# Performance work log

Measured on AMD Instinct MI355X. Metric: run time of the kernel, lower is better.

Reference implementation:

```python
import jax, jax.numpy as jnp
import numpy as np
from jax import lax

NMS_THRESH = 0.5
BN_EPS = 1e-5
TO_REMOVE = 1.0  # neural-motifs box convention (+1 in width/height)


def nms_overlaps(boxes):
    # boxes: [N, C, 4] xyxy -> per-class pairwise IoU [N, N, C]
    x1 = jnp.maximum(boxes[:, None, :, 0], boxes[None, :, :, 0])
    y1 = jnp.maximum(boxes[:, None, :, 1], boxes[None, :, :, 1])
    x2 = jnp.minimum(boxes[:, None, :, 2], boxes[None, :, :, 2])
    y2 = jnp.minimum(boxes[:, None, :, 3], boxes[None, :, :, 3])
    inter = jnp.clip(x2 - x1 + TO_REMOVE, 0.0) * jnp.clip(y2 - y1 + TO_REMOVE, 0.0)
    area = (boxes[:, :, 2] - boxes[:, :, 0] + TO_REMOVE) * (boxes[:, :, 3] - boxes[:, :, 1] + TO_REMOVE)  # [N,C]
    union = area[:, None, :] + area[None, :, :] - inter
    return inter / union


def greedy_nms_labels(obj_dists, is_overlap):
    # faithful port of nms_per_cls: iterative argmax + per-class suppression
    N, C = obj_dists.shape
    scores = jax.nn.softmax(obj_dists, axis=-1)
    scores = scores.at[:, 0].set(-1.0)  # kill background column

    def step(carry, _):
        scores, labels = carry
        flat = jnp.argmax(scores)          # row-major, same as np.unravel_index
        box_ind = flat // C
        cls_ind = flat % C
        labels = labels.at[box_ind].set(cls_ind.astype(jnp.int32))
        ov = is_overlap[box_ind, :, cls_ind]  # [N] bool
        col = jnp.where(ov, 0.0, scores[:, cls_ind])
        scores = scores.at[:, cls_ind].set(col)
        scores = scores.at[box_ind, :].set(-1.0)
        return (scores, labels), None

    (_, labels), _ = lax.scan(step, (scores, jnp.zeros(N, jnp.int32)), None, length=N)
    return labels


def setup_inputs() -> dict:
    key = jax.random.key(0)
    ks = jax.random.split(key, 16)
    N, C, D, E, H, P = 400, 151, 4096, 200, 512, 128
    x = jax.random.normal(ks[0], (N, D), jnp.float32)
    predict_logits = jax.random.normal(ks[1], (N, C), jnp.float32) * 2.0
    pos_input = jax.random.uniform(ks[2], (N, 9), jnp.float32)
    xy = jax.random.uniform(ks[3], (N, C, 2), jnp.float32) * 800.0
    wh = jax.random.uniform(ks[4], (N, C, 2), jnp.float32) * 200.0 + 1.0
    boxes_per_cls = jnp.concatenate([xy, xy + wh], axis=-1)
    sc = lambda k, sh: jax.random.normal(k, sh, jnp.float32) * np.float32(1.0 / np.sqrt(sh[0]))
    return {
        'x': x,
        'predict_logits': predict_logits,
        'pos_input': pos_input,
        'boxes_per_cls': boxes_per_cls,
        'obj_embed_w': jax.random.normal(ks[5], (C, E), jnp.float32) * 0.1,
        'obj_embed2_w': jax.random.normal(ks[6], (C, E), jnp.float32) * 0.1,
        'w_pos1': sc(ks[7], (9, 32)), 'b_pos1': jnp.zeros(32, jnp.float32),
        'bn_gamma': jnp.ones(32, jnp.float32), 'bn_beta': jnp.zeros(32, jnp.float32),
        'bn_mean': jnp.zeros(32, jnp.float32), 'bn_var': jnp.ones(32, jnp.float32),
        'w_pos2': sc(ks[8], (32, P)), 'b_pos2': jnp.zeros(P, jnp.float32),
        'w_lin': sc(ks[9], (D + E + P, H)), 'b_lin': jnp.zeros(H, jnp.float32),
        'w_out': sc(ks[10], (H, C)), 'b_out': jnp.zeros(C, jnp.float32),
        'w_fc': sc(ks[11], (D + E + P, H)), 'b_fc': jnp.zeros(H, jnp.float32),
    }


def reference(x, predict_logits, pos_input, boxes_per_cls, obj_embed_w, obj_embed2_w,
              w_pos1, b_pos1, bn_gamma, bn_beta, bn_mean, bn_var, w_pos2, b_pos2,
              w_lin, b_lin, w_out, b_out, w_fc, b_fc):
    # sgdet inference path of VTransEFeaturePE.forward
    obj_embed = jax.nn.softmax(predict_logits, axis=-1) @ obj_embed_w           # [N,E]
    h = pos_input @ w_pos1 + b_pos1                                             # Linear(9,32)
    h = (h - bn_mean) / jnp.sqrt(bn_var + BN_EPS) * bn_gamma + bn_beta          # BN eval
    pos_embed = jax.nn.relu(h @ w_pos2 + b_pos2)                                # [N,128]
    rep = jnp.concatenate([x, obj_embed, pos_embed], axis=-1)                   # [N,4424]
    obj_dists = (rep @ w_lin + b_lin) @ w_out + b_out                           # [N,C]
    is_overlap = nms_overlaps(boxes_per_cls) >= NMS_THRESH                      # [N,N,C]
    obj_preds = greedy_nms_labels(obj_dists, is_overlap)                        # [N] int32
    obj_embed2 = obj_embed2_w[obj_preds]                                        # [N,E]
    obj_rel_rep = jnp.concatenate([x, pos_embed, obj_embed2], axis=-1)
    edge_ctx = jax.nn.relu(obj_rel_rep @ w_fc + b_fc)                           # [N,H]
    return (obj_dists, obj_preds, edge_ctx)
```

## Files before the change

kernel.cpp:

```cpp
#include <hip/hip_runtime.h>
#include <hip/hip_bf16.h>
#include <stdint.h>

#define NB 400
#define NC 151
#define DX 4096
#define DE 200
#define DP 128
#define DH 512
#define KREP 4424
#define TAILW 328
#define MPAD 416
#define SPLITK 8
#define TILES1 139
#define TILES2 132
#define SLOTS 7
#define SKSTRIDE 152

__device__ __forceinline__ uint32_t f2ord(float f) {
  uint32_t u = __float_as_uint(f);
  return (u & 0x80000000u) ? ~u : (u | 0x80000000u);
}

__global__ __launch_bounds__(256) void k_embed(
    const float* __restrict__ logits, const float* __restrict__ obj_embed_w,
    const float* __restrict__ pos_input, const float* __restrict__ w_pos1,
    const float* __restrict__ b_pos1, const float* __restrict__ bn_gamma,
    const float* __restrict__ bn_beta, const float* __restrict__ bn_mean,
    const float* __restrict__ bn_var, const float* __restrict__ w_pos2,
    const float* __restrict__ b_pos2, float* __restrict__ tail1) {
  int r = blockIdx.x, t = threadIdx.x;
  if (r >= NB) {
    if (t < TAILW) tail1[r * TAILW + t] = 0.f;
    return;
  }
  __shared__ float p[NC];
  __shared__ float red[256];
  __shared__ float hb[32];

  float v = (t < NC) ? logits[r * NC + t] : -INFINITY;
  red[t] = v; __syncthreads();
  for (int s = 128; s > 0; s >>= 1) { if (t < s) red[t] = fmaxf(red[t], red[t + s]); __syncthreads(); }
  float m = red[0]; __syncthreads();
  float e = (t < NC) ? expf(v - m) : 0.f;
  red[t] = e; __syncthreads();
  for (int s = 128; s > 0; s >>= 1) { if (t < s) red[t] += red[t + s]; __syncthreads(); }
  float sum = red[0];
  if (t < NC) p[t] = e / sum;

  if (t < 32) {
    float acc = b_pos1[t];
    for (int k = 0; k < 9; k++) acc += pos_input[r * 9 + k] * w_pos1[k * 32 + t];
    acc = (acc - bn_mean[t]) / sqrtf(bn_var[t] + 1e-5f) * bn_gamma[t] + bn_beta[t];
    hb[t] = acc;
  }
  __syncthreads();

  if (t < DE) {
    float acc = 0.f;
    for (int k = 0; k < NC; k++) acc += p[k] * obj_embed_w[k * DE + t];
    tail1[r * TAILW + t] = acc;
  }
  if (t < DP) {
    float acc = b_pos2[t];
    for (int k = 0; k < 32; k++) acc += hb[k] * w_pos2[k * DP + t];
    tail1[r * TAILW + DE + t] = fmaxf(acc, 0.f);
  }
}

__device__ __forceinline__ void gemm_body(
    const float* __restrict__ x, const float* __restrict__ tail,
    const float* __restrict__ w, float* __restrict__ part,
    int bid, int tiles, int toff) {
  __shared__ __align__(16) float As[32][36];
  __shared__ __align__(16) float Bs[32][68];
  int tid = threadIdx.x;
  int n0 = (bid & 7) * 64, m0 = ((bid >> 3) % 13) * 32;
  int z = bid / 104;
  int tbeg = (z * tiles) / SPLITK, tend = ((z + 1) * tiles) / SPLITK;
  int ty = tid >> 4, tx = tid & 15;
  int a_r = tid >> 3, a_c = (tid & 7) << 2;
  int b_r = tid >> 4, b_c = (tid & 15) << 2;
  float4 acc0 = {0, 0, 0, 0}, acc1 = {0, 0, 0, 0};

  auto loadA = [&](int t) -> float4 {
    int k = t * 32 + a_c;
    int row = m0 + a_r;
    float4 v = {0, 0, 0, 0};
    if (k < KREP) {
      if (k < DX) { if (row < NB) v = *(const float4*)&x[(size_t)row * DX + k]; }
      else v = *(const float4*)&tail[row * TAILW + toff + (k - DX)];
    }
    return v;
  };
  auto loadB = [&](int t, int roff) -> float4 {
    int k = t * 32 + b_r + roff;
    float4 v = {0, 0, 0, 0};
    if (k < KREP) v = *(const float4*)&w[(size_t)k * DH + n0 + b_c];
    return v;
  };

  float4 pa = loadA(tbeg), pb0 = loadB(tbeg, 0), pb1 = loadB(tbeg, 16);
  for (int t = tbeg; t < tend; t++) {
    __syncthreads();
    *(float4*)&As[a_r][a_c] = pa;
    *(float4*)&Bs[b_r][b_c] = pb0;
    *(float4*)&Bs[b_r + 16][b_c] = pb1;
    __syncthreads();
    if (t + 1 < tend) { pa = loadA(t + 1); pb0 = loadB(t + 1, 0); pb1 = loadB(t + 1, 16); }
#pragma unroll
    for (int k4 = 0; k4 < 8; k4++) {
      float4 a0 = *(float4*)&As[ty * 2][k4 * 4];
      float4 a1 = *(float4*)&As[ty * 2 + 1][k4 * 4];
#pragma unroll
      for (int j = 0; j < 4; j++) {
        float4 bv = *(float4*)&Bs[k4 * 4 + j][tx * 4];
        float av0 = (&a0.x)[j], av1 = (&a1.x)[j];
        acc0.x += av0 * bv.x; acc0.y += av0 * bv.y; acc0.z += av0 * bv.z; acc0.w += av0 * bv.w;
        acc1.x += av1 * bv.x; acc1.y += av1 * bv.y; acc1.z += av1 * bv.z; acc1.w += av1 * bv.w;
      }
    }
  }
  int row0 = m0 + ty * 2, col = n0 + tx * 4;
  float* base = part + (size_t)z * NB * DH;
  if (row0 < NB)     *(float4*)&base[row0 * DH + col] = acc0;
  if (row0 + 1 < NB) *(float4*)&base[(row0 + 1) * DH + col] = acc1;
}

__global__ __launch_bounds__(256) void k_g1ov(
    const float* __restrict__ x, const float* __restrict__ tail1,
    const float* __restrict__ w_lin, float* __restrict__ part,
    const float* __restrict__ boxes, uint64_t* __restrict__ ov_bits) {
  int bid = blockIdx.x;
  if (bid >= 832) {
    int c = bid - 832;
    int t = threadIdx.x;
    __shared__ float4 bx[NB];
    const float4* bp4 = (const float4*)boxes;
    for (int j = t; j < NB; j += 256) bx[j] = bp4[j * NC + c];
    __syncthreads();
    int wave = t >> 6, lane = t & 63;
    for (int b = wave; b < NB; b += 4) {
      float4 A = bx[b];
      float areaA = (A.z - A.x + 1.f) * (A.w - A.y + 1.f);
      for (int chunk = 0; chunk < 7; chunk++) {
        int j = chunk * 64 + lane;
        bool ov = false;
        if (j < NB) {
          float4 B = bx[j];
          float x1 = fmaxf(A.x, B.x), y1 = fmaxf(A.y, B.y);
          float x2 = fminf(A.z, B.z), y2 = fminf(A.w, B.w);
          float iw = fmaxf(x2 - x1 + 1.f, 0.f), ih = fmaxf(y2 - y1 + 1.f, 0.f);
          float inter = iw * ih;
          float areaB = (B.z - B.x + 1.f) * (B.w - B.y + 1.f);
          ov = (inter / (areaA + areaB - inter)) >= 0.5f;
        }
        uint64_t mask = __ballot(ov);
        if (lane == 0) ov_bits[((size_t)(b * NC + c) << 3) + chunk] = mask;
      }
    }
    return;
  }
  gemm_body(x, tail1, w_lin, part, bid, TILES1, 0);
}

__global__ __launch_bounds__(256) void k_dists(
    const float* __restrict__ part, const float* __restrict__ b_lin,
    const float* __restrict__ w_out, const float* __restrict__ b_out,
    float* __restrict__ out_dists, uint64_t* __restrict__ skeys) {
  int r = blockIdx.x, t = threadIdx.x;
  __shared__ float h[DH];
  __shared__ float red[256];
  __shared__ float sval[NC];
  float s0 = b_lin[t], s1 = b_lin[t + 256];
#pragma unroll
  for (int z = 0; z < SPLITK; z++) {
    const float* pr = part + ((size_t)z * NB + r) * DH;
    s0 += pr[t]; s1 += pr[t + 256];
  }
  h[t] = s0; h[t + 256] = s1;
  __syncthreads();

  float acc = -INFINITY;
  if (t < NC) {
    acc = b_out[t];
    for (int k = 0; k < DH; k++) acc += h[k] * w_out[k * NC + t];
    out_dists[r * NC + t] = acc;
  }
  red[t] = (t < NC) ? acc : -INFINITY; __syncthreads();
  for (int s = 128; s > 0; s >>= 1) { if (t < s) red[t] = fmaxf(red[t], red[t + s]); __syncthreads(); }
  float mx = red[0]; __syncthreads();
  float e = (t < NC) ? expf(acc - mx) : 0.f;
  red[t] = e; __syncthreads();
  for (int s = 128; s > 0; s >>= 1) { if (t < s) red[t] += red[t + s]; __syncthreads(); }
  float sum = red[0];
  if (t < NC) sval[t] = e / sum;
  __syncthreads();

  if (t >= 1 && t < NC) {
    float v = sval[t];
    int rank = 0;
    for (int c2 = 1; c2 < NC; c2++) {
      float v2 = sval[c2];
      rank += (v2 > v) || (v2 == v && c2 < t);
    }
    skeys[(size_t)r * SKSTRIDE + rank] =
        ((uint64_t)f2ord(v) << 17) | ((uint64_t)(511 - r) << 8) | (uint64_t)t;
  }
}

__global__ __launch_bounds__(256) void k_nms_g2a(
    const uint64_t* __restrict__ ov_bits, const uint64_t* __restrict__ skeys,
    int* __restrict__ labels_g, float* __restrict__ out_preds,
    const float* __restrict__ x, const float* __restrict__ tail1,
    const float* __restrict__ w_fc, float* __restrict__ part) {
  if (blockIdx.x > 0) {
    gemm_body(x, tail1, w_fc, part, blockIdx.x - 1, TILES2, DE);
    return;
  }
  if (threadIdx.x >= 64) return;
  int lane = threadIdx.x;
  uint64_t cand[SLOTS];
  uint64_t supp0[SLOTS], supp1[SLOTS], supp2[SLOTS];
  int depth[SLOTS];
  bool removed[SLOTS];
  int reszmin[SLOTS];

#pragma unroll
  for (int s = 0; s < SLOTS; s++) {
    int r = s * 64 + lane;
    supp0[s] = supp1[s] = supp2[s] = 0;
    depth[s] = 0; removed[s] = false; reszmin[s] = 255;
    if (r < NB) {
      cand[s] = skeys[(size_t)r * SKSTRIDE];
      labels_g[r] = 0; out_preds[r] = 0.f;
    } else cand[s] = 0;
  }

  auto apply = [&](int b, int c, const uint64_t* ow) {
#pragma unroll
    for (int s = 0; s < SLOTS; s++) {
      int r = s * 64 + lane;
      if (r == b) {
        removed[s] = true; reszmin[s] = 255;
        cand[s] = ((uint64_t)0x407FFFFFu << 17) | ((uint64_t)(511 - r) << 8);
        labels_g[b] = c; out_preds[b] = (float)c;
      } else if ((ow[s] >> lane) & 1) {
        if (removed[s]) {
          if (c < reszmin[s]) reszmin[s] = c;
          cand[s] = ((uint64_t)0x80000000u << 17) | ((uint64_t)(511 - r) << 8)
                    | (uint64_t)reszmin[s];
        } else {
          uint64_t bit = 1ull << (c & 63);
          if (c < 64) supp0[s] |= bit; else if (c < 128) supp1[s] |= bit; else supp2[s] |= bit;
          if ((int)(cand[s] & 0xFF) == c) {
            int d = depth[s] + 1;
            uint64_t k = 0;
            for (; d < 150; d++) {
              k = skeys[(size_t)r * SKSTRIDE + d];
              int col = (int)(k & 0xFF);
              uint64_t mm = (col < 64) ? supp0[s] : ((col < 128) ? supp1[s] : supp2[s]);
              if (!((mm >> (col & 63)) & 1)) break;
            }
            if (d >= 150)
              k = ((uint64_t)0x80000000u << 17) | ((uint64_t)(511 - r) << 8) | 1ull;
            depth[s] = d; cand[s] = k;
          }
        }
      }
    }
  };

  auto cswap = [](uint64_t& a, uint64_t& b) {
    uint64_t hi = a > b ? a : b, lo = a > b ? b : a; a = hi; b = lo;
  };

  int picked = 0;
  while (picked < NB) {
    uint64_t k0 = 0, k1 = 0, k2 = 0, k3 = 0;
#pragma unroll
    for (int s = 0; s < SLOTS; s++) {
      uint64_t v = cand[s];
      if (v > k0)      { k3 = k2; k2 = k1; k1 = k0; k0 = v; }
      else if (v > k1) { k3 = k2; k2 = k1; k1 = v; }
      else if (v > k2) { k3 = k2; k2 = v; }
      else if (v > k3) { k3 = v; }
    }
#pragma unroll
    for (int off = 1; off < 64; off <<= 1) {
      uint64_t p0 = (uint64_t)__shfl_xor((unsigned long long)k0, off, 64);
      uint64_t p1 = (uint64_t)__shfl_xor((unsigned long long)k1, off, 64);
      uint64_t p2 = (uint64_t)__shfl_xor((unsigned long long)k2, off, 64);
      uint64_t p3 = (uint64_t)__shfl_xor((unsigned long long)k3, off, 64);
      uint64_t t0 = k0 > p3 ? k0 : p3;
      uint64_t t1 = k1 > p2 ? k1 : p2;
      uint64_t t2 = k2 > p1 ? k2 : p1;
      uint64_t t3 = k3 > p0 ? k3 : p0;
      cswap(t0, t2); cswap(t1, t3); cswap(t0, t1); cswap(t2, t3);
      k0 = t0; k1 = t1; k2 = t2; k3 = t3;
    }
    int b0 = 511 - (int)((k0 >> 8) & 0x1FF), c0 = (int)(k0 & 0xFF);
    int b1 = 511 - (int)((k1 >> 8) & 0x1FF), c1 = (int)(k1 & 0xFF);
    int b2 = 511 - (int)((k2 >> 8) & 0x1FF), c2 = (int)(k2 & 0xFF);
    int b3 = 511 - (int)((k3 >> 8) & 0x1FF), c3 = (int)(k3 & 0xFF);
    int npick = NB - picked; if (npick > 4) npick = 4;

    int pi = lane >> 3, pw = lane & 7;
    uint64_t wv = 0;
    if (pi < npick && pw < 7) {
      int bb = (pi == 0) ? b0 : (pi == 1) ? b1 : (pi == 2) ? b2 : b3;
      int cc = (pi == 0) ? c0 : (pi == 1) ? c1 : (pi == 2) ? c2 : c3;
      wv = ov_bits[(((size_t)(bb * NC + cc)) << 3) + pw];
    }
    auto ovb = [&](int ii, int bj) -> bool {
      bool f = ((lane >> 3) == ii) && ((lane & 7) == (bj >> 6)) && ((wv >> (bj & 63)) & 1);
      return __ballot(f) != 0ull;
    };
    uint32_t v1 = (uint32_t)(k1 >> 17), v2 = (uint32_t)(k2 >> 17), v3 = (uint32_t)(k3 >> 17);
    int napply = 1;
    if (npick >= 2 && v1 > 0x80000000u && !(c1 == c0 && ovb(0, b1))) {
      napply = 2;
      if (npick >= 3 && v2 > 0x80000000u &&
          !(c2 == c0 && ovb(0, b2)) && !(c2 == c1 && ovb(1, b2))) {
        napply = 3;
        if (npick >= 4 && v3 > 0x80000000u &&
            !(c3 == c0 && ovb(0, b3)) && !(c3 == c1 && ovb(1, b3)) &&
            !(c3 == c2 && ovb(2, b3)))
          napply = 4;
      }
    }

    uint64_t ow[SLOTS];
#pragma unroll
    for (int s = 0; s < SLOTS; s++) ow[s] = (uint64_t)__shfl((unsigned long long)wv, s, 64);
    apply(b0, c0, ow);
    if (napply >= 2) {
#pragma unroll
      for (int s = 0; s < SLOTS; s++) ow[s] = (uint64_t)__shfl((unsigned long long)wv, 8 + s, 64);
      apply(b1, c1, ow);
    }
    if (napply >= 3) {
#pragma unroll
      for (int s = 0; s < SLOTS; s++) ow[s] = (uint64_t)__shfl((unsigned long long)wv, 16 + s, 64);
      apply(b2, c2, ow);
    }
    if (napply >= 4) {
#pragma unroll
      for (int s = 0; s < SLOTS; s++) ow[s] = (uint64_t)__shfl((unsigned long long)wv, 24 + s, 64);
      apply(b3, c3, ow);
    }
    picked += napply;
  }
}

__global__ __launch_bounds__(256) void k_final(
    const float* __restrict__ emb2, const int* __restrict__ labels,
    const float* __restrict__ w_fc, const float* __restrict__ part,
    const float* __restrict__ b_fc, float* __restrict__ out_edge) {
  __shared__ __align__(16) float As[32][36];
  __shared__ __align__(16) float Bs[32][68];
  int tid = threadIdx.x;
  int n0 = blockIdx.x * 64, m0 = blockIdx.y * 32;
  int ty = tid >> 4, tx = tid & 15;
  int a_r = tid >> 3, a_c = (tid & 7) << 2;
  int b_r = tid >> 4, b_c = (tid & 15) << 2;
  float4 acc0 = {0, 0, 0, 0}, acc1 = {0, 0, 0, 0};
  int row_a = m0 + a_r;
  int lab = (row_a < NB) ? labels[row_a] : 0;

  auto loadA = [&](int t) -> float4 {
    int kk = t * 32 + a_c;
    float4 v = {0, 0, 0, 0};
    if (kk < DE && row_a < NB) v = *(const float4*)&emb2[(size_t)lab * DE + kk];
    return v;
  };
  auto loadB = [&](int t, int roff) -> float4 {
    int kk = t * 32 + b_r + roff;
    float4 v = {0, 0, 0, 0};
    if (kk < DE) v = *(const float4*)&w_fc[(size_t)(DX + DP + kk) * DH + n0 + b_c];
    return v;
  };

  float4 pa = loadA(0), pb0 = loadB(0, 0), pb1 = loadB(0, 16);
  for (int t = 0; t < 7; t++) {
    __syncthreads();
    *(float4*)&As[a_r][a_c] = pa;
    *(float4*)&Bs[b_r][b_c] = pb0;
    *(float4*)&Bs[b_r + 16][b_c] = pb1;
    __syncthreads();
    if (t + 1 < 7) { pa = loadA(t + 1); pb0 = loadB(t + 1, 0); pb1 = loadB(t + 1, 16); }
#pragma unroll
    for (int k4 = 0; k4 < 8; k4++) {
      float4 a0 = *(float4*)&As[ty * 2][k4 * 4];
      float4 a1 = *(float4*)&As[ty * 2 + 1][k4 * 4];
#pragma unroll
      for (int j = 0; j < 4; j++) {
        float4 bv = *(float4*)&Bs[k4 * 4 + j][tx * 4];
        float av0 = (&a0.x)[j], av1 = (&a1.x)[j];
        acc0.x += av0 * bv.x; acc0.y += av0 * bv.y; acc0.z += av0 * bv.z; acc0.w += av0 * bv.w;
        acc1.x += av1 * bv.x; acc1.y += av1 * bv.y; acc1.z += av1 * bv.z; acc1.w += av1 * bv.w;
      }
    }
  }
  int row0 = m0 + ty * 2, col = n0 + tx * 4;
#pragma unroll
  for (int z = 0; z < SPLITK; z++) {
    if (row0 < NB) {
      float4 p = *(const float4*)&part[((size_t)z * NB + row0) * DH + col];
      acc0.x += p.x; acc0.y += p.y; acc0.z += p.z; acc0.w += p.w;
    }
    if (row0 + 1 < NB) {
      float4 p = *(const float4*)&part[((size_t)z * NB + row0 + 1) * DH + col];
      acc1.x += p.x; acc1.y += p.y; acc1.z += p.z; acc1.w += p.w;
    }
  }
  float4 bv = *(const float4*)&b_fc[col];
  if (row0 < NB) {
    float4 r;
    r.x = fmaxf(acc0.x + bv.x, 0.f); r.y = fmaxf(acc0.y + bv.y, 0.f);
    r.z = fmaxf(acc0.z + bv.z, 0.f); r.w = fmaxf(acc0.w + bv.w, 0.f);
    *(float4*)&out_edge[row0 * DH + col] = r;
  }
  if (row0 + 1 < NB) {
    float4 r;
    r.x = fmaxf(acc1.x + bv.x, 0.f); r.y = fmaxf(acc1.y + bv.y, 0.f);
    r.z = fmaxf(acc1.z + bv.z, 0.f); r.w = fmaxf(acc1.w + bv.w, 0.f);
    *(float4*)&out_edge[(row0 + 1) * DH + col] = r;
  }
}

extern "C" void kernel_launch(void* const* d_in, const int* in_sizes, int n_in,
                              void* d_out, int out_size, void* d_ws, size_t ws_size,
                              hipStream_t stream) {
  const float* x            = (const float*)d_in[0];
  const float* logits       = (const float*)d_in[1];
  const float* pos_input    = (const float*)d_in[2];
  const float* boxes        = (const float*)d_in[3];
  const float* obj_embed_w  = (const float*)d_in[4];
  const float* obj_embed2_w = (const float*)d_in[5];
  const float* w_pos1       = (const float*)d_in[6];
  const float* b_pos1       = (const float*)d_in[7];
  const float* bn_gamma     = (const float*)d_in[8];
  const float* bn_beta      = (const float*)d_in[9];
  const float* bn_mean      = (const float*)d_in[10];
  const float* bn_var       = (const float*)d_in[11];
  const float* w_pos2       = (const float*)d_in[12];
  const float* b_pos2       = (const float*)d_in[13];
  const float* w_lin        = (const float*)d_in[14];
  const float* b_lin        = (const float*)d_in[15];
  const float* w_out        = (const float*)d_in[16];
  const float* b_out        = (const float*)d_in[17];
  const float* w_fc         = (const float*)d_in[18];
  const float* b_fc         = (const float*)d_in[19];

  float* ws         = (float*)d_ws;
  float* tail1      = ws;
  int* labels       = (int*)(tail1 + MPAD * TAILW);
  uint64_t* skeys   = (uint64_t*)(labels + MPAD);
  uint64_t* ov_bits = skeys + (size_t)NB * SKSTRIDE;
  float* part       = (float*)(ov_bits + (size_t)NB * NC * 8);

  float* out       = (float*)d_out;
  float* out_dists = out;
  float* out_preds = out + NB * NC;
  float* out_edge  = out + NB * NC + NB;

  k_embed<<<MPAD, 256, 0, stream>>>(logits, obj_embed_w, pos_input, w_pos1, b_pos1,
                                    bn_gamma, bn_beta, bn_mean, bn_var, w_pos2, b_pos2,
                                    tail1);
  k_g1ov<<<983, 256, 0, stream>>>(x, tail1, w_lin, part, boxes, ov_bits);
  k_dists<<<NB, 256, 0, stream>>>(part, b_lin, w_out, b_out, out_dists, skeys);
  k_nms_g2a<<<833, 256, 0, stream>>>(ov_bits, skeys, labels, out_preds,
                                     x, tail1, w_fc, part);
  k_final<<<dim3(8, 13), 256, 0, stream>>>(obj_embed2_w, labels, w_fc, part,
                                           b_fc, out_edge);
}
```

Before: 627.5 us.

## Widen greedy NMS to top-8 batched picks and halve GEMM tile width

The serial NMS wave now extracts the top 8 candidates per round with a sorting network and a 64-lane shuffle merge, up from 4. It stages the overlap rows in shared memory and moves the per-row suppression bitmasks from registers to LDS, so up to 8 non-conflicting picks can be applied per iteration and fewer serial rounds are needed. Separately, the split-K GEMM tile drops from 32x64 to 32x32, doubling the block count to 1664 for better CU fill alongside the long-running NMS block. The trade-offs are more sorting and shuffle work per round, LDS read-modify-write in the inner loop, and halved per-thread compute density in the GEMM.

```diff
diff --git a/kernel.cpp b/kernel.cpp
--- a/kernel.cpp
+++ b/kernel.cpp
@@ -16,6 +16,11 @@
 #define TILES2 132
 #define SLOTS 7
 #define SKSTRIDE 152
+#define NGB 1664
+
+#define CSW(x, y) do { uint64_t _hi = (x) > (y) ? (x) : (y); \
+                       uint64_t _lo = (x) > (y) ? (y) : (x); \
+                       (x) = _hi; (y) = _lo; } while (0)
 
 __device__ __forceinline__ uint32_t f2ord(float f) {
   uint32_t u = __float_as_uint(f);
@@ -73,15 +78,14 @@
     const float* __restrict__ w, float* __restrict__ part,
     int bid, int tiles, int toff) {
   __shared__ __align__(16) float As[32][36];
-  __shared__ __align__(16) float Bs[32][68];
+  __shared__ __align__(16) float Bs[32][36];
   int tid = threadIdx.x;
-  int n0 = (bid & 7) * 64, m0 = ((bid >> 3) % 13) * 32;
-  int z = bid / 104;
+  int n0 = (bid & 15) * 32, m0 = ((bid >> 4) % 13) * 32;
+  int z = bid / 208;
   int tbeg = (z * tiles) / SPLITK, tend = ((z + 1) * tiles) / SPLITK;
   int ty = tid >> 4, tx = tid & 15;
   int a_r = tid >> 3, a_c = (tid & 7) << 2;
-  int b_r = tid >> 4, b_c = (tid & 15) << 2;
-  float4 acc0 = {0, 0, 0, 0}, acc1 = {0, 0, 0, 0};
+  float acc00 = 0.f, acc01 = 0.f, acc10 = 0.f, acc11 = 0.f;
 
   auto loadA = [&](int t) -> float4 {
     int k = t * 32 + a_c;
@@ -93,38 +97,37 @@
     }
     return v;
   };
-  auto loadB = [&](int t, int roff) -> float4 {
-    int k = t * 32 + b_r + roff;
+  auto loadB = [&](int t) -> float4 {
+    int k = t * 32 + a_r;
     float4 v = {0, 0, 0, 0};
-    if (k < KREP) v = *(const float4*)&w[(size_t)k * DH + n0 + b_c];
+    if (k < KREP) v = *(const float4*)&w[(size_t)k * DH + n0 + a_c];
     return v;
   };
 
-  float4 pa = loadA(tbeg), pb0 = loadB(tbeg, 0), pb1 = loadB(tbeg, 16);
+  float4 pa = loadA(tbeg), pb = loadB(tbeg);
   for (int t = tbeg; t < tend; t++) {
     __syncthreads();
     *(float4*)&As[a_r][a_c] = pa;
-    *(float4*)&Bs[b_r][b_c] = pb0;
-    *(float4*)&Bs[b_r + 16][b_c] = pb1;
+    *(float4*)&Bs[a_r][a_c] = pb;
     __syncthreads();
-    if (t + 1 < tend) { pa = loadA(t + 1); pb0 = loadB(t + 1, 0); pb1 = loadB(t + 1, 16); }
+    if (t + 1 < tend) { pa = loadA(t + 1); pb = loadB(t + 1); }
 #pragma unroll
     for (int k4 = 0; k4 < 8; k4++) {
-      float4 a0 = *(float4*)&As[ty * 2][k4 * 4];
-      float4 a1 = *(float4*)&As[ty * 2 + 1][k4 * 4];
+      float4 av0 = *(float4*)&As[ty * 2][k4 * 4];
+      float4 av1 = *(float4*)&As[ty * 2 + 1][k4 * 4];
 #pragma unroll
       for (int j = 0; j < 4; j++) {
-        float4 bv = *(float4*)&Bs[k4 * 4 + j][tx * 4];
-        float av0 = (&a0.x)[j], av1 = (&a1.x)[j];
-        acc0.x += av0 * bv.x; acc0.y += av0 * bv.y; acc0.z += av0 * bv.z; acc0.w += av0 * bv.w;
-        acc1.x += av1 * bv.x; acc1.y += av1 * bv.y; acc1.z += av1 * bv.z; acc1.w += av1 * bv.w;
-      }
-    }
-  }
-  int row0 = m0 + ty * 2, col = n0 + tx * 4;
+        float2 bv = *(float2*)&Bs[k4 * 4 + j][tx * 2];
+        float x0 = (&av0.x)[j], x1 = (&av1.x)[j];
+        acc00 += x0 * bv.x; acc01 += x0 * bv.y;
+        acc10 += x1 * bv.x; acc11 += x1 * bv.y;
+      }
+    }
+  }
+  int row0 = m0 + ty * 2, col = n0 + tx * 2;
   float* base = part + (size_t)z * NB * DH;
-  if (row0 < NB)     *(float4*)&base[row0 * DH + col] = acc0;
-  if (row0 + 1 < NB) *(float4*)&base[(row0 + 1) * DH + col] = acc1;
+  if (row0 < NB)     { float2 v = {acc00, acc01}; *(float2*)&base[row0 * DH + col] = v; }
+  if (row0 + 1 < NB) { float2 v = {acc10, acc11}; *(float2*)&base[(row0 + 1) * DH + col] = v; }
 }
 
 __global__ __launch_bounds__(256) void k_g1ov(
@@ -132,8 +135,8 @@
     const float* __restrict__ w_lin, float* __restrict__ part,
     const float* __restrict__ boxes, uint64_t* __restrict__ ov_bits) {
   int bid = blockIdx.x;
-  if (bid >= 832) {
-    int c = bid - 832;
+  if (bid >= NGB) {
+    int c = bid - NGB;
     int t = threadIdx.x;
     __shared__ float4 bx[NB];
     const float4* bp4 = (const float4*)boxes;
@@ -218,136 +221,130 @@
     gemm_body(x, tail1, w_fc, part, blockIdx.x - 1, TILES2, DE);
     return;
   }
-  if (threadIdx.x >= 64) return;
-  int lane = threadIdx.x;
+  __shared__ uint64_t stageL[64];
+  __shared__ uint64_t suppL[448 * 3];
+
+  int tid = threadIdx.x;
+  for (int i = tid; i < 448 * 3; i += 256) suppL[i] = 0;
+  for (int r = tid; r < NB; r += 256) { labels_g[r] = 0; out_preds[r] = 0.f; }
+  __syncthreads();
+  if (tid >= 64) return;
+  int lane = tid;
+
+  const uint64_t SENTV = ((uint64_t)0x407FFFFFu << 17);
+  const uint64_t RESV  = ((uint64_t)0x80000000u << 17);
+
   uint64_t cand[SLOTS];
-  uint64_t supp0[SLOTS], supp1[SLOTS], supp2[SLOTS];
-  int depth[SLOTS];
-  bool removed[SLOTS];
-  int reszmin[SLOTS];
-
+  int depth[SLOTS], reszmin[SLOTS];
+  uint32_t remmask = 0;
 #pragma unroll
   for (int s = 0; s < SLOTS; s++) {
     int r = s * 64 + lane;
-    supp0[s] = supp1[s] = supp2[s] = 0;
-    depth[s] = 0; removed[s] = false; reszmin[s] = 255;
-    if (r < NB) {
-      cand[s] = skeys[(size_t)r * SKSTRIDE];
-      labels_g[r] = 0; out_preds[r] = 0.f;
-    } else cand[s] = 0;
-  }
-
-  auto apply = [&](int b, int c, const uint64_t* ow) {
+    cand[s] = (r < NB) ? skeys[(size_t)r * SKSTRIDE] : 0;
+    depth[s] = 0; reszmin[s] = 255;
+  }
+
+  int picked = 0;
+  while (picked < NB) {
+    uint64_t a[8];
+#pragma unroll
+    for (int s = 0; s < SLOTS; s++) a[s] = cand[s];
+    a[7] = 0;
+#pragma unroll
+    for (int rd = 0; rd < 7; rd++) {
+      if (rd & 1) { CSW(a[1], a[2]); CSW(a[3], a[4]); CSW(a[5], a[6]); }
+      else        { CSW(a[0], a[1]); CSW(a[2], a[3]); CSW(a[4], a[5]); }
+    }
+#pragma unroll
+    for (int off = 1; off < 64; off <<= 1) {
+      uint64_t p[8], t8[8];
+#pragma unroll
+      for (int i = 0; i < 8; i++)
+        p[i] = (uint64_t)__shfl_xor((unsigned long long)a[i], off, 64);
+#pragma unroll
+      for (int i = 0; i < 8; i++) { uint64_t q = p[7 - i]; t8[i] = a[i] > q ? a[i] : q; }
+      CSW(t8[0], t8[4]); CSW(t8[1], t8[5]); CSW(t8[2], t8[6]); CSW(t8[3], t8[7]);
+      CSW(t8[0], t8[2]); CSW(t8[1], t8[3]); CSW(t8[4], t8[6]); CSW(t8[5], t8[7]);
+      CSW(t8[0], t8[1]); CSW(t8[2], t8[3]); CSW(t8[4], t8[5]); CSW(t8[6], t8[7]);
+#pragma unroll
+      for (int i = 0; i < 8; i++) a[i] = t8[i];
+    }
+    int bb[8], cc[8];
+#pragma unroll
+    for (int i = 0; i < 8; i++) {
+      bb[i] = 511 - (int)((a[i] >> 8) & 0x1FF);
+      cc[i] = (int)(a[i] & 0xFF);
+    }
+    int npick = NB - picked; if (npick > 8) npick = 8;
+
+    int pi = lane >> 3, pw = lane & 7;
+    if (pi < npick && pw < 7)
+      stageL[(pi << 3) + pw] = ov_bits[(((size_t)(bb[pi] * NC + cc[pi])) << 3) + pw];
+
+    int napply = 1;
+    for (int j = 1; j < 8; j++) {
+      if (j >= npick) break;
+      if ((uint32_t)(a[j] >> 17) <= 0x80000000u) break;
+      bool ok = true;
+      for (int i = 0; i < j; i++) {
+        if (cc[i] == cc[j]) {
+          uint64_t wv = stageL[(i << 3) + (bb[j] >> 6)];
+          if ((wv >> (bb[j] & 63)) & 1) ok = false;
+        }
+      }
+      if (!ok) break;
+      napply = j + 1;
+    }
+
 #pragma unroll
     for (int s = 0; s < SLOTS; s++) {
       int r = s * 64 + lane;
-      if (r == b) {
-        removed[s] = true; reszmin[s] = 255;
-        cand[s] = ((uint64_t)0x407FFFFFu << 17) | ((uint64_t)(511 - r) << 8);
-        labels_g[b] = c; out_preds[b] = (float)c;
-      } else if ((ow[s] >> lane) & 1) {
-        if (removed[s]) {
-          if (c < reszmin[s]) reszmin[s] = c;
-          cand[s] = ((uint64_t)0x80000000u << 17) | ((uint64_t)(511 - r) << 8)
-                    | (uint64_t)reszmin[s];
-        } else {
-          uint64_t bit = 1ull << (c & 63);
-          if (c < 64) supp0[s] |= bit; else if (c < 128) supp1[s] |= bit; else supp2[s] |= bit;
-          if ((int)(cand[s] & 0xFF) == c) {
-            int d = depth[s] + 1;
-            uint64_t k = 0;
-            for (; d < 150; d++) {
-              k = skeys[(size_t)r * SKSTRIDE + d];
-              int col = (int)(k & 0xFF);
-              uint64_t mm = (col < 64) ? supp0[s] : ((col < 128) ? supp1[s] : supp2[s]);
-              if (!((mm >> (col & 63)) & 1)) break;
+      uint64_t w[8];
+#pragma unroll
+      for (int i = 0; i < 8; i++) w[i] = (i < napply) ? stageL[(i << 3) + s] : 0;
+      uint64_t cv = cand[s];
+      bool rem = (remmask >> s) & 1;
+      int rm = reszmin[s], dp = depth[s];
+#pragma unroll
+      for (int i = 0; i < 8; i++) {
+        if (i >= napply) break;
+        int b = bb[i], c = cc[i];
+        if (r == b) {
+          rem = true; rm = 255;
+          cv = SENTV | ((uint64_t)(511 - r) << 8);
+        } else if ((w[i] >> lane) & 1) {
+          if (rem) {
+            if (c < rm) rm = c;
+            cv = RESV | ((uint64_t)(511 - r) << 8) | (uint64_t)rm;
+          } else {
+            int wo = c >> 6;
+            uint64_t sb = suppL[r * 3 + wo] | (1ull << (c & 63));
+            suppL[r * 3 + wo] = sb;
+            if ((int)(cv & 0xFF) == c) {
+              int d = dp + 1;
+              uint64_t nk = 0;
+              for (; d < 150; d++) {
+                nk = skeys[(size_t)r * SKSTRIDE + d];
+                int col = (int)(nk & 0xFF);
+                uint64_t m = suppL[r * 3 + (col >> 6)];
+                if (!((m >> (col & 63)) & 1)) break;
+              }
+              if (d >= 150)
+                nk = RESV | ((uint64_t)(511 - r) << 8) | 1ull;
+              dp = d; cv = nk;
             }
-            if (d >= 150)
-              k = ((uint64_t)0x80000000u << 17) | ((uint64_t)(511 - r) << 8) | 1ull;
-            depth[s] = d; cand[s] = k;
           }
         }
       }
-    }
-  };
-
-  auto cswap = [](uint64_t& a, uint64_t& b) {
-    uint64_t hi = a > b ? a : b, lo = a > b ? b : a; a = hi; b = lo;
-  };
-
-  int picked = 0;
-  while (picked < NB) {
-    uint64_t k0 = 0, k1 = 0, k2 = 0, k3 = 0;
-#pragma unroll
-    for (int s = 0; s < SLOTS; s++) {
-      uint64_t v = cand[s];
-      if (v > k0)      { k3 = k2; k2 = k1; k1 = k0; k0 = v; }
-      else if (v > k1) { k3 = k2; k2 = k1; k1 = v; }
-      else if (v > k2) { k3 = k2; k2 = v; }
-      else if (v > k3) { k3 = v; }
-    }
-#pragma unroll
-    for (int off = 1; off < 64; off <<= 1) {
-      uint64_t p0 = (uint64_t)__shfl_xor((unsigned long long)k0, off, 64);
-      uint64_t p1 = (uint64_t)__shfl_xor((unsigned long long)k1, off, 64);
-      uint64_t p2 = (uint64_t)__shfl_xor((unsigned long long)k2, off, 64);
-      uint64_t p3 = (uint64_t)__shfl_xor((unsigned long long)k3, off, 64);
-      uint64_t t0 = k0 > p3 ? k0 : p3;
-      uint64_t t1 = k1 > p2 ? k1 : p2;
-      uint64_t t2 = k2 > p1 ? k2 : p1;
-      uint64_t t3 = k3 > p0 ? k3 : p0;
-      cswap(t0, t2); cswap(t1, t3); cswap(t0, t1); cswap(t2, t3);
-      k0 = t0; k1 = t1; k2 = t2; k3 = t3;
-    }
-    int b0 = 511 - (int)((k0 >> 8) & 0x1FF), c0 = (int)(k0 & 0xFF);
-    int b1 = 511 - (int)((k1 >> 8) & 0x1FF), c1 = (int)(k1 & 0xFF);
-    int b2 = 511 - (int)((k2 >> 8) & 0x1FF), c2 = (int)(k2 & 0xFF);
-    int b3 = 511 - (int)((k3 >> 8) & 0x1FF), c3 = (int)(k3 & 0xFF);
-    int npick = NB - picked; if (npick > 4) npick = 4;
-
-    int pi = lane >> 3, pw = lane & 7;
-    uint64_t wv = 0;
-    if (pi < npick && pw < 7) {
-      int bb = (pi == 0) ? b0 : (pi == 1) ? b1 : (pi == 2) ? b2 : b3;
-      int cc = (pi == 0) ? c0 : (pi == 1) ? c1 : (pi == 2) ? c2 : c3;
-      wv = ov_bits[(((size_t)(bb * NC + cc)) << 3) + pw];
-    }
-    auto ovb = [&](int ii, int bj) -> bool {
-      bool f = ((lane >> 3) == ii) && ((lane & 7) == (bj >> 6)) && ((wv >> (bj & 63)) & 1);
-      return __ballot(f) != 0ull;
-    };
-    uint32_t v1 = (uint32_t)(k1 >> 17), v2 = (uint32_t)(k2 >> 17), v3 = (uint32_t)(k3 >> 17);
-    int napply = 1;
-    if (npick >= 2 && v1 > 0x80000000u && !(c1 == c0 && ovb(0, b1))) {
-      napply = 2;
-      if (npick >= 3 && v2 > 0x80000000u &&
-          !(c2 == c0 && ovb(0, b2)) && !(c2 == c1 && ovb(1, b2))) {
-        napply = 3;
-        if (npick >= 4 && v3 > 0x80000000u &&
-            !(c3 == c0 && ovb(0, b3)) && !(c3 == c1 && ovb(1, b3)) &&
-            !(c3 == c2 && ovb(2, b3)))
-          napply = 4;
-      }
-    }
-
-    uint64_t ow[SLOTS];
-#pragma unroll
-    for (int s = 0; s < SLOTS; s++) ow[s] = (uint64_t)__shfl((unsigned long long)wv, s, 64);
-    apply(b0, c0, ow);
-    if (napply >= 2) {
-#pragma unroll
-      for (int s = 0; s < SLOTS; s++) ow[s] = (uint64_t)__shfl((unsigned long long)wv, 8 + s, 64);
-      apply(b1, c1, ow);
-    }
-    if (napply >= 3) {
-#pragma unroll
-      for (int s = 0; s < SLOTS; s++) ow[s] = (uint64_t)__shfl((unsigned long long)wv, 16 + s, 64);
-      apply(b2, c2, ow);
-    }
-    if (napply >= 4) {
-#pragma unroll
-      for (int s = 0; s < SLOTS; s++) ow[s] = (uint64_t)__shfl((unsigned long long)wv, 24 + s, 64);
-      apply(b3, c3, ow);
+      cand[s] = cv; reszmin[s] = rm; depth[s] = dp;
+      if (rem) remmask |= (1u << s);
+    }
+#pragma unroll
+    for (int i = 0; i < 8; i++) {
+      if (i < napply && lane == i) {
+        labels_g[bb[i]] = cc[i];
+        out_preds[bb[i]] = (float)cc[i];
+      }
     }
     picked += napply;
   }
@@ -468,10 +465,10 @@
   k_embed<<<MPAD, 256, 0, stream>>>(logits, obj_embed_w, pos_input, w_pos1, b_pos1,
                                     bn_gamma, bn_beta, bn_mean, bn_var, w_pos2, b_pos2,
                                     tail1);
-  k_g1ov<<<983, 256, 0, stream>>>(x, tail1, w_lin, part, boxes, ov_bits);
+  k_g1ov<<<NGB + NC, 256, 0, stream>>>(x, tail1, w_lin, part, boxes, ov_bits);
   k_dists<<<NB, 256, 0, stream>>>(part, b_lin, w_out, b_out, out_dists, skeys);
-  k_nms_g2a<<<833, 256, 0, stream>>>(ov_bits, skeys, labels, out_preds,
-                                     x, tail1, w_fc, part);
+  k_nms_g2a<<<NGB + 1, 256, 0, stream>>>(ov_bits, skeys, labels, out_preds,
+                                         x, tail1, w_fc, part);
   k_final<<<dim3(8, 13), 256, 0, stream>>>(obj_embed2_w, labels, w_fc, part,
                                            b_fc, out_edge);
 }
```

Result: slower. 836.3 us (+33.3%).

## Replace per-row candidate NMS with global sorted-key sweep via histogram bin sort

Applied to the files above, without the earlier changes.

Greedy NMS no longer keeps per-row candidate heaps with top-4 wave merges. All 60000 (box, class) score keys are now globally sorted with a histogram, prefix scan, scatter and per-bin bitonic sort, and a single wave sweeps them in order while tracking suppression bitmasks in shared memory. A fallback loop handles rows whose classes are all suppressed and rows already removed. This is meant to cut the serial dependency chain of the greedy loop, at the cost of three extra kernel launches, global atomics, and a serial insertion sort if any bin holds more than 1024 keys.

```diff
diff --git a/kernel.cpp b/kernel.cpp
--- a/kernel.cpp
+++ b/kernel.cpp
@@ -14,8 +14,9 @@
 #define SPLITK 8
 #define TILES1 139
 #define TILES2 132
-#define SLOTS 7
-#define SKSTRIDE 152
+#define NGB 832
+#define NBINS 65536
+#define NKEYS 60000
 
 __device__ __forceinline__ uint32_t f2ord(float f) {
   uint32_t u = __float_as_uint(f);
@@ -28,8 +29,11 @@
     const float* __restrict__ b_pos1, const float* __restrict__ bn_gamma,
     const float* __restrict__ bn_beta, const float* __restrict__ bn_mean,
     const float* __restrict__ bn_var, const float* __restrict__ w_pos2,
-    const float* __restrict__ b_pos2, float* __restrict__ tail1) {
+    const float* __restrict__ b_pos2, float* __restrict__ tail1,
+    uint32_t* __restrict__ hist) {
   int r = blockIdx.x, t = threadIdx.x;
+  int gid = r * 256 + t;
+  if (gid < NBINS) hist[gid] = 0;
   if (r >= NB) {
     if (t < TAILW) tail1[r * TAILW + t] = 0.f;
     return;
@@ -71,9 +75,7 @@
 __device__ __forceinline__ void gemm_body(
     const float* __restrict__ x, const float* __restrict__ tail,
     const float* __restrict__ w, float* __restrict__ part,
-    int bid, int tiles, int toff) {
-  __shared__ __align__(16) float As[32][36];
-  __shared__ __align__(16) float Bs[32][68];
+    int bid, int tiles, int toff, float* As, float* Bs) {
   int tid = threadIdx.x;
   int n0 = (bid & 7) * 64, m0 = ((bid >> 3) % 13) * 32;
   int z = bid / 104;
@@ -103,18 +105,18 @@
   float4 pa = loadA(tbeg), pb0 = loadB(tbeg, 0), pb1 = loadB(tbeg, 16);
   for (int t = tbeg; t < tend; t++) {
     __syncthreads();
-    *(float4*)&As[a_r][a_c] = pa;
-    *(float4*)&Bs[b_r][b_c] = pb0;
-    *(float4*)&Bs[b_r + 16][b_c] = pb1;
+    *(float4*)&As[a_r * 36 + a_c] = pa;
+    *(float4*)&Bs[b_r * 68 + b_c] = pb0;
+    *(float4*)&Bs[(b_r + 16) * 68 + b_c] = pb1;
     __syncthreads();
     if (t + 1 < tend) { pa = loadA(t + 1); pb0 = loadB(t + 1, 0); pb1 = loadB(t + 1, 16); }
 #pragma unroll
     for (int k4 = 0; k4 < 8; k4++) {
-      float4 a0 = *(float4*)&As[ty * 2][k4 * 4];
-      float4 a1 = *(float4*)&As[ty * 2 + 1][k4 * 4];
+      float4 a0 = *(float4*)&As[(ty * 2) * 36 + k4 * 4];
+      float4 a1 = *(float4*)&As[(ty * 2 + 1) * 36 + k4 * 4];
 #pragma unroll
       for (int j = 0; j < 4; j++) {
-        float4 bv = *(float4*)&Bs[k4 * 4 + j][tx * 4];
+        float4 bv = *(float4*)&Bs[(k4 * 4 + j) * 68 + tx * 4];
         float av0 = (&a0.x)[j], av1 = (&a1.x)[j];
         acc0.x += av0 * bv.x; acc0.y += av0 * bv.y; acc0.z += av0 * bv.z; acc0.w += av0 * bv.w;
         acc1.x += av1 * bv.x; acc1.y += av1 * bv.y; acc1.z += av1 * bv.z; acc1.w += av1 * bv.w;
@@ -131,11 +133,12 @@
     const float* __restrict__ x, const float* __restrict__ tail1,
     const float* __restrict__ w_lin, float* __restrict__ part,
     const float* __restrict__ boxes, uint64_t* __restrict__ ov_bits) {
+  __shared__ __align__(16) char pool[13312];
   int bid = blockIdx.x;
-  if (bid >= 832) {
-    int c = bid - 832;
+  if (bid >= NGB) {
+    int c = bid - NGB;
     int t = threadIdx.x;
-    __shared__ float4 bx[NB];
+    float4* bx = (float4*)pool;
     const float4* bp4 = (const float4*)boxes;
     for (int j = t; j < NB; j += 256) bx[j] = bp4[j * NC + c];
     __syncthreads();
@@ -161,17 +164,18 @@
     }
     return;
   }
-  gemm_body(x, tail1, w_lin, part, bid, TILES1, 0);
+  gemm_body(x, tail1, w_lin, part, bid, TILES1, 0,
+            (float*)pool, (float*)(pool + 4608));
 }
 
 __global__ __launch_bounds__(256) void k_dists(
     const float* __restrict__ part, const float* __restrict__ b_lin,
     const float* __restrict__ w_out, const float* __restrict__ b_out,
-    float* __restrict__ out_dists, uint64_t* __restrict__ skeys) {
+    float* __restrict__ out_dists, uint64_t* __restrict__ ukeys,
+    uint32_t* __restrict__ hist) {
   int r = blockIdx.x, t = threadIdx.x;
   __shared__ float h[DH];
   __shared__ float red[256];
-  __shared__ float sval[NC];
   float s0 = b_lin[t], s1 = b_lin[t + 256];
 #pragma unroll
   for (int z = 0; z < SPLITK; z++) {
@@ -194,162 +198,228 @@
   red[t] = e; __syncthreads();
   for (int s = 128; s > 0; s >>= 1) { if (t < s) red[t] += red[t + s]; __syncthreads(); }
   float sum = red[0];
-  if (t < NC) sval[t] = e / sum;
+
+  if (t >= 1 && t < NC) {
+    float v = e / sum;
+    uint64_t key = ((uint64_t)f2ord(v) << 17) | ((uint64_t)(511 - r) << 8) | (uint64_t)t;
+    ukeys[r * 150 + (t - 1)] = key;
+    atomicAdd(&hist[NBINS - 1 - (uint32_t)(key >> 33)], 1u);
+  }
+}
+
+__global__ __launch_bounds__(1024) void k_sps(
+    const uint32_t* __restrict__ hist, uint32_t* __restrict__ bases,
+    uint32_t* __restrict__ cursor) {
+  __shared__ uint32_t tsum[1024];
+  int t = threadIdx.x;
+  uint32_t s = 0;
+  for (int i = 0; i < 64; i++) s += hist[t * 64 + i];
+  tsum[t] = s;
   __syncthreads();
-
-  if (t >= 1 && t < NC) {
-    float v = sval[t];
-    int rank = 0;
-    for (int c2 = 1; c2 < NC; c2++) {
-      float v2 = sval[c2];
-      rank += (v2 > v) || (v2 == v && c2 < t);
-    }
-    skeys[(size_t)r * SKSTRIDE + rank] =
-        ((uint64_t)f2ord(v) << 17) | ((uint64_t)(511 - r) << 8) | (uint64_t)t;
+  for (int off = 1; off < 1024; off <<= 1) {
+    uint32_t v = (t >= off) ? tsum[t - off] : 0;
+    __syncthreads();
+    tsum[t] += v;
+    __syncthreads();
+  }
+  uint32_t run = tsum[t] - s;
+  for (int i = 0; i < 64; i++) {
+    uint32_t hh = hist[t * 64 + i];
+    bases[t * 64 + i] = run;
+    cursor[t * 64 + i] = run;
+    run += hh;
+  }
+  if (t == 1023) bases[NBINS] = run;
+}
+
+__global__ __launch_bounds__(256) void k_scatter(
+    const uint64_t* __restrict__ ukeys, uint32_t* __restrict__ cursor,
+    uint64_t* __restrict__ gkeys) {
+  int i = blockIdx.x * 256 + threadIdx.x;
+  if (i < NKEYS) {
+    uint64_t key = ukeys[i];
+    uint32_t bin = NBINS - 1 - (uint32_t)(key >> 33);
+    uint32_t pos = atomicAdd(&cursor[bin], 1u);
+    gkeys[pos] = key;
+  } else if (i < NKEYS + 64) {
+    gkeys[i] = 0;
+  }
+}
+
+__global__ __launch_bounds__(256) void k_binsort(
+    const uint32_t* __restrict__ bases, uint64_t* __restrict__ gkeys) {
+  __shared__ uint64_t buf[1024];
+  __shared__ uint32_t bbase[257];
+  int tid = threadIdx.x;
+  int b0 = blockIdx.x * 256;
+  for (int i = tid; i < 257; i += 256) bbase[i] = bases[b0 + i];
+  __syncthreads();
+  for (int bi = 0; bi < 256; bi++) {
+    int lo = (int)bbase[bi], n = (int)bbase[bi + 1] - lo;
+    if (n < 2) continue;
+    if (n <= 1024) {
+      int p2 = 1; while (p2 < n) p2 <<= 1;
+      for (int i = tid; i < p2; i += 256) buf[i] = (i < n) ? gkeys[lo + i] : 0;
+      __syncthreads();
+      for (int k = 2; k <= p2; k <<= 1) {
+        for (int j = k >> 1; j > 0; j >>= 1) {
+          for (int i = tid; i < p2; i += 256) {
+            int ix = i ^ j;
+            if (ix > i) {
+              uint64_t av = buf[i], bv = buf[ix];
+              bool desc = ((i & k) == 0);
+              if (desc ? (av < bv) : (av > bv)) { buf[i] = bv; buf[ix] = av; }
+            }
+          }
+          __syncthreads();
+        }
+      }
+      for (int i = tid; i < n; i += 256) gkeys[lo + i] = buf[i];
+      __syncthreads();
+    } else {
+      if (tid == 0) {
+        for (int a = 1; a < n; a++) {
+          uint64_t k = gkeys[lo + a];
+          int b = a - 1;
+          while (b >= 0 && gkeys[lo + b] < k) { gkeys[lo + b + 1] = gkeys[lo + b]; b--; }
+          gkeys[lo + b + 1] = k;
+        }
+      }
+      __syncthreads();
+    }
   }
 }
 
 __global__ __launch_bounds__(256) void k_nms_g2a(
-    const uint64_t* __restrict__ ov_bits, const uint64_t* __restrict__ skeys,
+    const uint64_t* __restrict__ ov_bits, const uint64_t* __restrict__ gkeys,
     int* __restrict__ labels_g, float* __restrict__ out_preds,
     const float* __restrict__ x, const float* __restrict__ tail1,
     const float* __restrict__ w_fc, float* __restrict__ part) {
+  __shared__ __align__(16) char pool[13312];
   if (blockIdx.x > 0) {
-    gemm_body(x, tail1, w_fc, part, blockIdx.x - 1, TILES2, DE);
+    gemm_body(x, tail1, w_fc, part, blockIdx.x - 1, TILES2, DE,
+              (float*)pool, (float*)(pool + 4608));
     return;
   }
-  if (threadIdx.x >= 64) return;
-  int lane = threadIdx.x;
-  uint64_t cand[SLOTS];
-  uint64_t supp0[SLOTS], supp1[SLOTS], supp2[SLOTS];
-  int depth[SLOTS];
-  bool removed[SLOTS];
-  int reszmin[SLOTS];
-
-#pragma unroll
-  for (int s = 0; s < SLOTS; s++) {
-    int r = s * 64 + lane;
-    supp0[s] = supp1[s] = supp2[s] = 0;
-    depth[s] = 0; removed[s] = false; reszmin[s] = 255;
-    if (r < NB) {
-      cand[s] = skeys[(size_t)r * SKSTRIDE];
-      labels_g[r] = 0; out_preds[r] = 0.f;
-    } else cand[s] = 0;
-  }
-
-  auto apply = [&](int b, int c, const uint64_t* ow) {
-#pragma unroll
-    for (int s = 0; s < SLOTS; s++) {
+  uint64_t* suppL = (uint64_t*)pool;
+  uint32_t* reszL = (uint32_t*)(pool + 10752);
+  int tid = threadIdx.x;
+  if (tid >= 64) return;
+  int lane = tid;
+  for (int i = lane; i < 448 * 3; i += 64) suppL[i] = 0;
+  for (int i = lane; i < 448; i += 64) reszL[i] = 255u;
+  for (int r = lane; r < NB; r += 64) { labels_g[r] = 0; out_preds[r] = 0.f; }
+  uint64_t rem[7] = {0, 0, 0, 0, 0, 0, 0};
+
+  int picked = 0, pos = 0;
+  while (picked < NB && pos < NKEYS) {
+    int i = pos + lane;
+    uint64_t key = gkeys[i];
+    bool hask = (key != 0) && (i < NKEYS);
+    int r = hask ? (511 - (int)((key >> 8) & 0x1FF)) : 0;
+    int c = hask ? (int)(key & 0xFF) : 0;
+    const uint64_t* prow = ov_bits + (((size_t)(r * NC + c)) << 3);
+    uint64_t pf[7];
+#pragma unroll
+    for (int k = 0; k < 7; k++) pf[k] = prow[k];
+    bool valid = hask;
+    if (valid) {
+      uint64_t rb = 0;
+#pragma unroll
+      for (int s = 0; s < 7; s++) if (s == (r >> 6)) rb = rem[s];
+      valid = !((rb >> (r & 63)) & 1);
+    }
+    if (valid) {
+      uint64_t sb = suppL[r * 3 + (c >> 6)];
+      valid = !((sb >> (c & 63)) & 1);
+    }
+    uint64_t live = __ballot(valid);
+    while (live != 0 && picked < NB) {
+      int p = __ffsll((unsigned long long)live) - 1;
+      uint64_t kp = (uint64_t)__shfl((unsigned long long)key, p, 64);
+      int rp = 511 - (int)((kp >> 8) & 0x1FF);
+      int cp = (int)(kp & 0xFF);
+      uint64_t ow[7];
+#pragma unroll
+      for (int k = 0; k < 7; k++)
+        ow[k] = (uint64_t)__shfl((unsigned long long)pf[k], p, 64);
+      if (lane == p) { labels_g[rp] = cp; out_preds[rp] = (float)cp; }
+#pragma unroll
+      for (int s = 0; s < 7; s++) if (s == (rp >> 6)) rem[s] |= (1ull << (rp & 63));
+#pragma unroll
+      for (int s = 0; s < 7; s++) {
+        if ((ow[s] >> lane) & 1) {
+          int rr = s * 64 + lane;
+          if (rr != rp && rr < NB) {
+            if ((rem[s] >> lane) & 1) {
+              if ((uint32_t)cp < reszL[rr]) reszL[rr] = (uint32_t)cp;
+            } else {
+              suppL[rr * 3 + (cp >> 6)] |= (1ull << (cp & 63));
+            }
+          }
+        }
+      }
+      if (valid) {
+        if (r == rp) valid = false;
+        else if (c == cp) {
+          uint64_t w2 = 0;
+#pragma unroll
+          for (int s = 0; s < 7; s++) if (s == (r >> 6)) w2 = ow[s];
+          if ((w2 >> (r & 63)) & 1) valid = false;
+        }
+      }
+      if (lane == p) valid = false;
+      picked++;
+      live = __ballot(valid);
+    }
+    pos += 64;
+  }
+
+  while (picked < NB) {
+    uint32_t best = 0xFFFFFFFFu;
+#pragma unroll
+    for (int s = 0; s < 7; s++) {
       int r = s * 64 + lane;
-      if (r == b) {
-        removed[s] = true; reszmin[s] = 255;
-        cand[s] = ((uint64_t)0x407FFFFFu << 17) | ((uint64_t)(511 - r) << 8);
-        labels_g[b] = c; out_preds[b] = (float)c;
-      } else if ((ow[s] >> lane) & 1) {
-        if (removed[s]) {
-          if (c < reszmin[s]) reszmin[s] = c;
-          cand[s] = ((uint64_t)0x80000000u << 17) | ((uint64_t)(511 - r) << 8)
-                    | (uint64_t)reszmin[s];
+      if (r < NB) {
+        uint32_t cand = 0xFFFFFFFFu;
+        if ((rem[s] >> lane) & 1) {
+          uint32_t z = reszL[r];
+          if (z < 255u) cand = (uint32_t)(r * NC) + z;
         } else {
-          uint64_t bit = 1ull << (c & 63);
-          if (c < 64) supp0[s] |= bit; else if (c < 128) supp1[s] |= bit; else supp2[s] |= bit;
-          if ((int)(cand[s] & 0xFF) == c) {
-            int d = depth[s] + 1;
-            uint64_t k = 0;
-            for (; d < 150; d++) {
-              k = skeys[(size_t)r * SKSTRIDE + d];
-              int col = (int)(k & 0xFF);
-              uint64_t mm = (col < 64) ? supp0[s] : ((col < 128) ? supp1[s] : supp2[s]);
-              if (!((mm >> (col & 63)) & 1)) break;
-            }
-            if (d >= 150)
-              k = ((uint64_t)0x80000000u << 17) | ((uint64_t)(511 - r) << 8) | 1ull;
-            depth[s] = d; cand[s] = k;
+          int pc = __popcll(suppL[r * 3]) + __popcll(suppL[r * 3 + 1]) +
+                   __popcll(suppL[r * 3 + 2]);
+          if (pc >= 150) cand = (uint32_t)(r * NC) + 1u;
+        }
+        if (cand < best) best = cand;
+      }
+    }
+    for (int off = 1; off < 64; off <<= 1) {
+      uint32_t o = (uint32_t)__shfl_xor((int)best, off, 64);
+      if (o < best) best = o;
+    }
+    if (best == 0xFFFFFFFFu) break;
+    int rp = (int)(best / NC), cp = (int)(best % NC);
+    uint64_t wv = (lane < 7) ? ov_bits[(((size_t)(rp * NC + cp)) << 3) + lane] : 0;
+    uint64_t ow[7];
+#pragma unroll
+    for (int k = 0; k < 7; k++) ow[k] = (uint64_t)__shfl((unsigned long long)wv, k, 64);
+    if (lane == 0) { labels_g[rp] = cp; out_preds[rp] = (float)cp; reszL[rp] = 255u; }
+#pragma unroll
+    for (int s = 0; s < 7; s++) if (s == (rp >> 6)) rem[s] |= (1ull << (rp & 63));
+#pragma unroll
+    for (int s = 0; s < 7; s++) {
+      if ((ow[s] >> lane) & 1) {
+        int rr = s * 64 + lane;
+        if (rr != rp && rr < NB) {
+          if ((rem[s] >> lane) & 1) {
+            if ((uint32_t)cp < reszL[rr]) reszL[rr] = (uint32_t)cp;
+          } else {
+            suppL[rr * 3 + (cp >> 6)] |= (1ull << (cp & 63));
           }
         }
       }
     }
-  };
-
-  auto cswap = [](uint64_t& a, uint64_t& b) {
-    uint64_t hi = a > b ? a : b, lo = a > b ? b : a; a = hi; b = lo;
-  };
-
-  int picked = 0;
-  while (picked < NB) {
-    uint64_t k0 = 0, k1 = 0, k2 = 0, k3 = 0;
-#pragma unroll
-    for (int s = 0; s < SLOTS; s++) {
-      uint64_t v = cand[s];
-      if (v > k0)      { k3 = k2; k2 = k1; k1 = k0; k0 = v; }
-      else if (v > k1) { k3 = k2; k2 = k1; k1 = v; }
-      else if (v > k2) { k3 = k2; k2 = v; }
-      else if (v > k3) { k3 = v; }
-    }
-#pragma unroll
-    for (int off = 1; off < 64; off <<= 1) {
-      uint64_t p0 = (uint64_t)__shfl_xor((unsigned long long)k0, off, 64);
-      uint64_t p1 = (uint64_t)__shfl_xor((unsigned long long)k1, off, 64);
-      uint64_t p2 = (uint64_t)__shfl_xor((unsigned long long)k2, off, 64);
-      uint64_t p3 = (uint64_t)__shfl_xor((unsigned long long)k3, off, 64);
-      uint64_t t0 = k0 > p3 ? k0 : p3;
-      uint64_t t1 = k1 > p2 ? k1 : p2;
-      uint64_t t2 = k2 > p1 ? k2 : p1;
-      uint64_t t3 = k3 > p0 ? k3 : p0;
-      cswap(t0, t2); cswap(t1, t3); cswap(t0, t1); cswap(t2, t3);
-      k0 = t0; k1 = t1; k2 = t2; k3 = t3;
-    }
-    int b0 = 511 - (int)((k0 >> 8) & 0x1FF), c0 = (int)(k0 & 0xFF);
-    int b1 = 511 - (int)((k1 >> 8) & 0x1FF), c1 = (int)(k1 & 0xFF);
-    int b2 = 511 - (int)((k2 >> 8) & 0x1FF), c2 = (int)(k2 & 0xFF);
-    int b3 = 511 - (int)((k3 >> 8) & 0x1FF), c3 = (int)(k3 & 0xFF);
-    int npick = NB - picked; if (npick > 4) npick = 4;
-
-    int pi = lane >> 3, pw = lane & 7;
-    uint64_t wv = 0;
-    if (pi < npick && pw < 7) {
-      int bb = (pi == 0) ? b0 : (pi == 1) ? b1 : (pi == 2) ? b2 : b3;
-      int cc = (pi == 0) ? c0 : (pi == 1) ? c1 : (pi == 2) ? c2 : c3;
-      wv = ov_bits[(((size_t)(bb * NC + cc)) << 3) + pw];
-    }
-    auto ovb = [&](int ii, int bj) -> bool {
-      bool f = ((lane >> 3) == ii) && ((lane & 7) == (bj >> 6)) && ((wv >> (bj & 63)) & 1);
-      return __ballot(f) != 0ull;
-    };
-    uint32_t v1 = (uint32_t)(k1 >> 17), v2 = (uint32_t)(k2 >> 17), v3 = (uint32_t)(k3 >> 17);
-    int napply = 1;
-    if (npick >= 2 && v1 > 0x80000000u && !(c1 == c0 && ovb(0, b1))) {
-      napply = 2;
-      if (npick >= 3 && v2 > 0x80000000u &&
-          !(c2 == c0 && ovb(0, b2)) && !(c2 == c1 && ovb(1, b2))) {
-        napply = 3;
-        if (npick >= 4 && v3 > 0x80000000u &&
-            !(c3 == c0 && ovb(0, b3)) && !(c3 == c1 && ovb(1, b3)) &&
-            !(c3 == c2 && ovb(2, b3)))
-          napply = 4;
-      }
-    }
-
-    uint64_t ow[SLOTS];
-#pragma unroll
-    for (int s = 0; s < SLOTS; s++) ow[s] = (uint64_t)__shfl((unsigned long long)wv, s, 64);
-    apply(b0, c0, ow);
-    if (napply >= 2) {
-#pragma unroll
-      for (int s = 0; s < SLOTS; s++) ow[s] = (uint64_t)__shfl((unsigned long long)wv, 8 + s, 64);
-      apply(b1, c1, ow);
-    }
-    if (napply >= 3) {
-#pragma unroll
-      for (int s = 0; s < SLOTS; s++) ow[s] = (uint64_t)__shfl((unsigned long long)wv, 16 + s, 64);
-      apply(b2, c2, ow);
-    }
-    if (napply >= 4) {
-#pragma unroll
-      for (int s = 0; s < SLOTS; s++) ow[s] = (uint64_t)__shfl((unsigned long long)wv, 24 + s, 64);
-      apply(b3, c3, ow);
-    }
-    picked += napply;
+    picked++;
   }
 }
 
@@ -453,12 +523,16 @@
   const float* w_fc         = (const float*)d_in[18];
   const float* b_fc         = (const float*)d_in[19];
 
-  float* ws         = (float*)d_ws;
-  float* tail1      = ws;
-  int* labels       = (int*)(tail1 + MPAD * TAILW);
-  uint64_t* skeys   = (uint64_t*)(labels + MPAD);
-  uint64_t* ov_bits = skeys + (size_t)NB * SKSTRIDE;
-  float* part       = (float*)(ov_bits + (size_t)NB * NC * 8);
+  char* wp = (char*)d_ws;
+  float* tail1      = (float*)wp;  wp += (size_t)MPAD * TAILW * 4;
+  int* labels       = (int*)wp;    wp += 512 * 4;
+  uint32_t* hist    = (uint32_t*)wp; wp += (size_t)NBINS * 4;
+  uint32_t* bases   = (uint32_t*)wp; wp += (size_t)(NBINS + 4) * 4;
+  uint32_t* cursor  = (uint32_t*)wp; wp += (size_t)NBINS * 4;
+  uint64_t* ukeys   = (uint64_t*)wp; wp += (size_t)60032 * 8;
+  uint64_t* gkeys   = (uint64_t*)wp; wp += (size_t)60032 * 8;
+  uint64_t* ov_bits = (uint64_t*)wp; wp += (size_t)NB * NC * 8 * 8;
+  float* part       = (float*)wp;
 
   float* out       = (float*)d_out;
   float* out_dists = out;
@@ -467,11 +541,14 @@
 
   k_embed<<<MPAD, 256, 0, stream>>>(logits, obj_embed_w, pos_input, w_pos1, b_pos1,
                                     bn_gamma, bn_beta, bn_mean, bn_var, w_pos2, b_pos2,
-                                    tail1);
-  k_g1ov<<<983, 256, 0, stream>>>(x, tail1, w_lin, part, boxes, ov_bits);
-  k_dists<<<NB, 256, 0, stream>>>(part, b_lin, w_out, b_out, out_dists, skeys);
-  k_nms_g2a<<<833, 256, 0, stream>>>(ov_bits, skeys, labels, out_preds,
-                                     x, tail1, w_fc, part);
+                                    tail1, hist);
+  k_g1ov<<<NGB + NC, 256, 0, stream>>>(x, tail1, w_lin, part, boxes, ov_bits);
+  k_dists<<<NB, 256, 0, stream>>>(part, b_lin, w_out, b_out, out_dists, ukeys, hist);
+  k_sps<<<1, 1024, 0, stream>>>(hist, bases, cursor);
+  k_scatter<<<236, 256, 0, stream>>>(ukeys, cursor, gkeys);
+  k_binsort<<<256, 256, 0, stream>>>(bases, gkeys);
+  k_nms_g2a<<<NGB + 1, 256, 0, stream>>>(ov_bits, gkeys, labels, out_preds,
+                                         x, tail1, w_fc, part);
   k_final<<<dim3(8, 13), 256, 0, stream>>>(obj_embed2_w, labels, w_fc, part,
                                            b_fc, out_edge);
 }
```

New measurement: 2.218 ms. 3.53x slower.
